# Kernel tuning notes

Hardware: AMD Instinct MI355X
Metric: run time of the kernel (lower is better)

Reference implementation:

```python
import jax, jax.numpy as jnp
import numpy as np

ALPHA = 0.7
N = 4194304
NUM_ACTIONS = 3


def setup_inputs() -> dict:
    key = jax.random.key(0)
    k1, k2, k3, k4, k5 = jax.random.split(key, 5)
    return {
        "pred_prices": jax.random.normal(k1, (N,), dtype=jnp.float32),
        "pred_actions": jax.random.normal(k2, (N, NUM_ACTIONS), dtype=jnp.float32),
        "tgt_prices": jax.random.normal(k3, (N,), dtype=jnp.float32),
        "tgt_actions": jax.random.randint(k4, (N,), 0, NUM_ACTIONS, dtype=jnp.int64),
        "prices": jax.random.normal(k5, (N,), dtype=jnp.float32),
    }


def reference(pred_prices, pred_actions, tgt_prices, tgt_actions, prices):
    # MSE over price predictions
    price_loss = jnp.mean((pred_prices - tgt_prices) ** 2)

    # Cross-entropy (mean over batch), matches nn.CrossEntropyLoss on logits
    logp = jax.nn.log_softmax(pred_actions, axis=-1)  # [N, 3]
    action_loss = -jnp.mean(jnp.take_along_axis(logp, tgt_actions[:, None], axis=-1))

    # Vectorized replacement of the per-sample profit loop (no_grad in original)
    predicted_actions = jnp.argmax(pred_actions, axis=-1)  # [N]
    p = tgt_prices
    d = p[1:] - p[:-1]                     # [N-1]
    zero = jnp.zeros((1,), p.dtype)
    diff_fwd = jnp.concatenate([d, zero])  # p[i+1]-p[i], last entry 0
    diff_bwd = jnp.concatenate([zero, d])  # p[i]-p[i-1], first entry 0
    profits = jnp.where(predicted_actions == 0, diff_fwd,
                        jnp.where(predicted_actions == 2, diff_bwd,
                                  jnp.zeros_like(p)))
    profit_weight = jax.nn.sigmoid(profits * 10.0)
    weighted_action_loss = action_loss * jnp.mean(profit_weight)

    return ALPHA * weighted_action_loss + (1.0 - ALPHA) * price_loss
```

## Files before the change

### kernel.cpp

```cpp
#include <hip/hip_runtime.h>

static constexpr int NN  = 4194304;
static constexpr int NB  = 1024;
static constexpr int TPB = 256;
static constexpr int GPT = 4;

__global__ __launch_bounds__(256) void pfl_main(
    const float* __restrict__ pp,
    const float* __restrict__ pa,
    const float* __restrict__ tp,
    const int*   __restrict__ ta,
    float* __restrict__ bsum)
{
    const int tid  = threadIdx.x;
    const int bid  = blockIdx.x;
    const int base = bid * (TPB * GPT);
    const int lane = tid & 63;

    const float4* pp4 = (const float4*)pp;
    const float4* tp4 = (const float4*)tp;
    const float4* pa4 = (const float4*)pa;
    const int4*   ta4 = (const int4*)ta;

    float4 p[GPT], t[GPT], A0[GPT], A1[GPT], A2[GPT];
    int4   a[GPT];
    #pragma unroll
    for (int k = 0; k < GPT; ++k) {
        const int g = base + k * TPB + tid;
        p[k]  = pp4[g];
        t[k]  = tp4[g];
        a[k]  = ta4[g];
        A0[k] = pa4[3*g + 0];
        A1[k] = pa4[3*g + 1];
        A2[k] = pa4[3*g + 2];
    }

    float sq = 0.f, ce = 0.f, pw = 0.f;

    #pragma unroll
    for (int k = 0; k < GPT; ++k) {
        const int g = base + k * TPB + tid;
        const int i = g * 4;

        float tm1 = __shfl_up(t[k].w, 1, 64);
        float tnx = __shfl_down(t[k].x, 1, 64);
        if (lane == 0)  tm1 = (i > 0)      ? tp[i - 1] : 0.f;
        if (lane == 63) tnx = (i + 4 < NN) ? tp[i + 4] : 0.f;

        float tv[6] = {tm1, t[k].x, t[k].y, t[k].z, t[k].w, tnx};
        float pv[4] = {p[k].x, p[k].y, p[k].z, p[k].w};
        float rows[4][3] = {{A0[k].x, A0[k].y, A0[k].z},
                            {A0[k].w, A1[k].x, A1[k].y},
                            {A1[k].z, A1[k].w, A2[k].x},
                            {A2[k].y, A2[k].z, A2[k].w}};
        int av[4] = {a[k].x, a[k].y, a[k].z, a[k].w};

        #pragma unroll
        for (int j = 0; j < 4; ++j) {
            const int idx = i + j;
            float d = pv[j] - tv[j + 1];
            sq += d * d;

            float x0 = rows[j][0], x1 = rows[j][1], x2 = rows[j][2];
            float m  = fmaxf(x0, fmaxf(x1, x2));
            float lse = m + __logf(__expf(x0 - m) + __expf(x1 - m) + __expf(x2 - m));
            float tgt = (av[j] == 0) ? x0 : ((av[j] == 1) ? x1 : x2);
            ce += lse - tgt;

            int pidx = 0;
            float best = x0;
            if (x1 > best) { best = x1; pidx = 1; }
            if (x2 > best) { pidx = 2; }

            float profit = 0.f;
            if (pidx == 0)      profit = (idx + 1 < NN) ? (tv[j + 2] - tv[j + 1]) : 0.f;
            else if (pidx == 2) profit = (idx > 0)      ? (tv[j + 1] - tv[j])     : 0.f;

            pw += 1.f / (1.f + __expf(-10.f * profit));
        }
    }

    #pragma unroll
    for (int off = 32; off > 0; off >>= 1) {
        sq += __shfl_down(sq, off, 64);
        ce += __shfl_down(ce, off, 64);
        pw += __shfl_down(pw, off, 64);
    }

    __shared__ float s_sq[4], s_ce[4], s_pw[4];
    const int wid = tid >> 6;
    if (lane == 0) { s_sq[wid] = sq; s_ce[wid] = ce; s_pw[wid] = pw; }
    __syncthreads();

    if (tid == 0) {
        bsum[bid]          = s_sq[0] + s_sq[1] + s_sq[2] + s_sq[3];
        bsum[NB + bid]     = s_ce[0] + s_ce[1] + s_ce[2] + s_ce[3];
        bsum[2 * NB + bid] = s_pw[0] + s_pw[1] + s_pw[2] + s_pw[3];
    }
}

__global__ __launch_bounds__(256) void pfl_final(const float* __restrict__ bsum,
                                                 float* __restrict__ out) {
    const int tid = threadIdx.x;
    const float4* b4 = (const float4*)bsum;
    const int Q = NB / 4;

    float4 vsq = b4[tid];
    float4 vce = b4[Q + tid];
    float4 vpw = b4[2 * Q + tid];

    double sq = (double)vsq.x + vsq.y + vsq.z + vsq.w;
    double ce = (double)vce.x + vce.y + vce.z + vce.w;
    double pw = (double)vpw.x + vpw.y + vpw.z + vpw.w;

    #pragma unroll
    for (int off = 32; off > 0; off >>= 1) {
        sq += __shfl_down(sq, off, 64);
        ce += __shfl_down(ce, off, 64);
        pw += __shfl_down(pw, off, 64);
    }

    __shared__ double s_sq[4], s_ce[4], s_pw[4];
    const int lane = tid & 63;
    const int wid  = tid >> 6;
    if (lane == 0) { s_sq[wid] = sq; s_ce[wid] = ce; s_pw[wid] = pw; }
    __syncthreads();

    if (tid == 0) {
        double tsq = s_sq[0] + s_sq[1] + s_sq[2] + s_sq[3];
        double tce = s_ce[0] + s_ce[1] + s_ce[2] + s_ce[3];
        double tpw = s_pw[0] + s_pw[1] + s_pw[2] + s_pw[3];
        const double inv = 1.0 / (double)NN;
        out[0] = (float)(0.7 * (tce * inv) * (tpw * inv) + 0.3 * (tsq * inv));
    }
}

extern "C" void kernel_launch(void* const* d_in, const int* in_sizes, int n_in,
                              void* d_out, int out_size, void* d_ws, size_t ws_size,
                              hipStream_t stream) {
    const float* pp = (const float*)d_in[0];
    const float* pa = (const float*)d_in[1];
    const float* tp = (const float*)d_in[2];
    const int*   ta = (const int*)d_in[3];

    float* bsum = (float*)d_ws;

    pfl_main<<<NB, TPB, 0, stream>>>(pp, pa, tp, ta, bsum);
    pfl_final<<<1, TPB, 0, stream>>>(bsum, (float*)d_out);
}
```

Measured before the change: 137.8 us.

## Double-buffer grid-strided loads and fetch neighbor prices directly

Changes the per-thread work from four contiguous chunks loaded all up front to a grid-stride pattern with two-slot register double buffering, issuing the next chunk's loads before computing the current one. Neighbor prices at the chunk edges are now loaded by every thread straight from memory instead of passed by wavefront shuffles. The aim is to cut register pressure and overlap load latency with compute. The cost is two extra scalar loads per chunk, mostly served from cache, and possibly less memory-level parallelism than issuing all loads at once.

Measured after the change: 137.6 us. About the same (-0.1%).

```diff
diff --git a/kernel.cpp b/kernel.cpp
--- a/kernel.cpp
+++ b/kernel.cpp
@@ -1,9 +1,10 @@
 #include <hip/hip_runtime.h>
 
-static constexpr int NN  = 4194304;
-static constexpr int NB  = 1024;
-static constexpr int TPB = 256;
-static constexpr int GPT = 4;
+static constexpr int NN   = 4194304;
+static constexpr int NB   = 1024;
+static constexpr int TPB  = 256;
+static constexpr int ITER = 4;
+static constexpr int STRIDE = NB * TPB;
 
 __global__ __launch_bounds__(256) void pfl_main(
     const float* __restrict__ pp,
@@ -14,46 +15,60 @@
 {
     const int tid  = threadIdx.x;
     const int bid  = blockIdx.x;
-    const int base = bid * (TPB * GPT);
-    const int lane = tid & 63;
+    const int g0   = bid * TPB + tid;
 
     const float4* pp4 = (const float4*)pp;
     const float4* tp4 = (const float4*)tp;
     const float4* pa4 = (const float4*)pa;
     const int4*   ta4 = (const int4*)ta;
 
-    float4 p[GPT], t[GPT], A0[GPT], A1[GPT], A2[GPT];
-    int4   a[GPT];
-    #pragma unroll
-    for (int k = 0; k < GPT; ++k) {
-        const int g = base + k * TPB + tid;
-        p[k]  = pp4[g];
-        t[k]  = tp4[g];
-        a[k]  = ta4[g];
-        A0[k] = pa4[3*g + 0];
-        A1[k] = pa4[3*g + 1];
-        A2[k] = pa4[3*g + 2];
+    float4 P[2], T[2], B0[2], B1[2], B2[2];
+    int4   A[2];
+    float  TM[2], TX[2];
+
+    {
+        const int g = g0;
+        const int i = g * 4;
+        P[0]  = pp4[g];
+        T[0]  = tp4[g];
+        A[0]  = ta4[g];
+        B0[0] = pa4[3*g + 0];
+        B1[0] = pa4[3*g + 1];
+        B2[0] = pa4[3*g + 2];
+        TM[0] = (i > 0)      ? tp[i - 1] : 0.f;
+        TX[0] = (i + 4 < NN) ? tp[i + 4] : 0.f;
     }
 
     float sq = 0.f, ce = 0.f, pw = 0.f;
 
     #pragma unroll
-    for (int k = 0; k < GPT; ++k) {
-        const int g = base + k * TPB + tid;
+    for (int k = 0; k < ITER; ++k) {
+        const int cur = k & 1;
+        const int nxt = cur ^ 1;
+
+        if (k + 1 < ITER) {
+            const int g = g0 + (k + 1) * STRIDE;
+            const int i = g * 4;
+            P[nxt]  = pp4[g];
+            T[nxt]  = tp4[g];
+            A[nxt]  = ta4[g];
+            B0[nxt] = pa4[3*g + 0];
+            B1[nxt] = pa4[3*g + 1];
+            B2[nxt] = pa4[3*g + 2];
+            TM[nxt] = (i > 0)      ? tp[i - 1] : 0.f;
+            TX[nxt] = (i + 4 < NN) ? tp[i + 4] : 0.f;
+        }
+
+        const int g = g0 + k * STRIDE;
         const int i = g * 4;
 
-        float tm1 = __shfl_up(t[k].w, 1, 64);
-        float tnx = __shfl_down(t[k].x, 1, 64);
-        if (lane == 0)  tm1 = (i > 0)      ? tp[i - 1] : 0.f;
-        if (lane == 63) tnx = (i + 4 < NN) ? tp[i + 4] : 0.f;
-
-        float tv[6] = {tm1, t[k].x, t[k].y, t[k].z, t[k].w, tnx};
-        float pv[4] = {p[k].x, p[k].y, p[k].z, p[k].w};
-        float rows[4][3] = {{A0[k].x, A0[k].y, A0[k].z},
-                            {A0[k].w, A1[k].x, A1[k].y},
-                            {A1[k].z, A1[k].w, A2[k].x},
-                            {A2[k].y, A2[k].z, A2[k].w}};
-        int av[4] = {a[k].x, a[k].y, a[k].z, a[k].w};
+        float tv[6] = {TM[cur], T[cur].x, T[cur].y, T[cur].z, T[cur].w, TX[cur]};
+        float pv[4] = {P[cur].x, P[cur].y, P[cur].z, P[cur].w};
+        float rows[4][3] = {{B0[cur].x, B0[cur].y, B0[cur].z},
+                            {B0[cur].w, B1[cur].x, B1[cur].y},
+                            {B1[cur].z, B1[cur].w, B2[cur].x},
+                            {B2[cur].y, B2[cur].z, B2[cur].w}};
+        int av[4] = {A[cur].x, A[cur].y, A[cur].z, A[cur].w};
 
         #pragma unroll
         for (int j = 0; j < 4; ++j) {
@@ -88,7 +103,8 @@
     }
 
     __shared__ float s_sq[4], s_ce[4], s_pw[4];
-    const int wid = tid >> 6;
+    const int lane = tid & 63;
+    const int wid  = tid >> 6;
     if (lane == 0) { s_sq[wid] = sq; s_ce[wid] = ce; s_pw[wid] = pw; }
     __syncthreads();
 
```
